# Performance work log

Hardware: AMD Instinct MI355X
Metric: run time of the kernel (lower is better)

## Reference

```python
import jax, jax.numpy as jnp
import numpy as np

B, D, S = 16384, 1024, 2048
LN_EPS = 1e-5


def setup_inputs() -> dict:
    key = jax.random.key(0)
    ks = jax.random.split(key, 16)
    inv_d = 1.0 / np.sqrt(D)
    inv_s = 1.0 / np.sqrt(S)
    inv_ds = 1.0 / np.sqrt(D + S)
    return {
        "x_t": jax.random.normal(ks[0], (B, D), jnp.float32),
        "state": jax.random.normal(ks[1], (B, S), jnp.float32),
        "conditioning": jax.random.normal(ks[2], (B, D), jnp.float32),
        "carry_scale": jax.random.uniform(ks[3], (B, S), jnp.float32),
        # Linear weights stored [in, out] (y = x @ W + b); equivalent math to torch's x @ W.T
        "W_step": jax.random.normal(ks[4], (D, S), jnp.float32) * inv_d,
        "b_step": jnp.zeros((S,), jnp.float32),
        "W_cstep": jax.random.normal(ks[5], (D, S), jnp.float32) * inv_d,
        "W_in": jax.random.normal(ks[6], (D, S), jnp.float32) * inv_d,
        "b_in": jnp.zeros((S,), jnp.float32),
        "W_cin": jax.random.normal(ks[7], (D, S), jnp.float32) * inv_d,
        "W_state": jax.random.normal(ks[8], (S, S), jnp.float32) * inv_s,
        "W_out": jax.random.normal(ks[9], (D + S, D), jnp.float32) * inv_ds,
        "b_out": jnp.zeros((D,), jnp.float32),
        "ln_w": jnp.ones((D,), jnp.float32),
        "ln_b": jnp.zeros((D,), jnp.float32),
        "log_decay": jnp.zeros((S,), jnp.float32),
    }


def reference(x_t, state, conditioning, carry_scale,
              W_step, b_step, W_cstep, W_in, b_in, W_cin,
              W_state, W_out, b_out, ln_w, ln_b, log_decay):
    # input-conditioned step size
    step = jax.nn.softplus(x_t @ W_step + b_step)
    step = step + 0.1 * jax.nn.softplus(conditioning @ W_cstep)
    # candidate state
    proposal = jnp.tanh(x_t @ W_in + b_in + conditioning @ W_cin + state @ W_state)
    # diagonal decay gate
    decay = jnp.exp(-step * jnp.exp(log_decay)) * carry_scale
    new_state = decay * state + (1.0 - decay) * proposal
    # output projection + residual LayerNorm
    out = jnp.concatenate([x_t, new_state], axis=-1) @ W_out + b_out
    h = out + x_t
    mu = jnp.mean(h, axis=-1, keepdims=True)
    var = jnp.mean(jnp.square(h - mu), axis=-1, keepdims=True)
    output = (h - mu) * jax.lax.rsqrt(var + LN_EPS) * ln_w + ln_b
    return output, new_state
```

## Files before the change

kernel.cpp:

```cpp
#include <hip/hip_runtime.h>
#include <hip/hip_bf16.h>
#include <cstdint>
#include <cstddef>

#define BB 16384
#define DD 1024
#define SS 2048

typedef __attribute__((ext_vector_type(8))) short s8vec;
typedef __attribute__((ext_vector_type(4))) short s4vec;
typedef __attribute__((ext_vector_type(4))) float f4vec;

static __device__ __forceinline__ short f2bf(float x) {
  __hip_bfloat16 h = __float2bfloat16(x);
  union { __hip_bfloat16 b; short s; } u; u.b = h; return u.s;
}

static __device__ __forceinline__ float softplus_f(float x) {
  return (x > 20.f) ? x : log1pf(expf(x));
}

static __device__ __forceinline__ void gload16(const void* g, void* l) {
  __builtin_amdgcn_global_load_lds((__attribute__((address_space(1))) void*)g,
                                   (__attribute__((address_space(3))) void*)l,
                                   16, 0, 0);
}

struct EpiParams {
  float* out;
  const float* bias;
  const float* step;
  const float* state;
  const float* carry;
  const float* ldec;
  float* out_state;
  short* xy;
  const float* x;
};

template<int EPI>
__global__ __launch_bounds__(256)
void gemm_bt(const short* __restrict__ A, int lda,
             const short* __restrict__ Bt, int ldb,
             int K, EpiParams ep)
{
  __shared__ short Alds[128 * 32];
  __shared__ short Blds[128 * 32];

  const int tid  = threadIdx.x;
  const int lane = tid & 63;
  const int wv   = tid >> 6;
  const int bm   = blockIdx.y;
  const int bn   = blockIdx.x;

  const int srow = wv * 32 + (lane >> 2);
  const int scol = (lane & 3) * 8;
  const short* Ag = A  + (size_t)(bm * 128 + srow) * lda + scol;
  const short* Bg = Bt + (size_t)(bn * 128 + srow) * ldb + scol;
  short* Al = &Alds[(wv * 32) * 32] + lane * 8;
  short* Bl = &Blds[(wv * 32) * 32] + lane * 8;

  const int wM = (wv >> 1) * 64;
  const int wN = (wv & 1) * 64;
  const int frow = lane & 15;
  const int fk   = (lane >> 4) * 8;

  f4vec acc[4][4];
#pragma unroll
  for (int i = 0; i < 4; i++)
#pragma unroll
    for (int j = 0; j < 4; j++) acc[i][j] = (f4vec){0.f, 0.f, 0.f, 0.f};

  for (int k0 = 0; k0 < K; k0 += 32) {
    __syncthreads();
    gload16(Ag + k0,            Al);
    gload16(Ag + k0 + 16 * lda, Al + 16 * 32);
    gload16(Bg + k0,            Bl);
    gload16(Bg + k0 + 16 * ldb, Bl + 16 * 32);
    __syncthreads();

    s8vec a[4], b[4];
#pragma unroll
    for (int i = 0; i < 4; i++)
      a[i] = *(const s8vec*)&Alds[(wM + i * 16 + frow) * 32 + fk];
#pragma unroll
    for (int j = 0; j < 4; j++)
      b[j] = *(const s8vec*)&Blds[(wN + j * 16 + frow) * 32 + fk];

#pragma unroll
    for (int i = 0; i < 4; i++)
#pragma unroll
      for (int j = 0; j < 4; j++)
        acc[i][j] = __builtin_amdgcn_mfma_f32_16x16x32_bf16(a[i], b[j], acc[i][j], 0, 0, 0);
  }

  const int erow = bm * 128 + wM + (lane >> 4) * 4;
  const int ecol = bn * 128 + wN + (lane & 15);

#pragma unroll
  for (int i = 0; i < 4; i++) {
#pragma unroll
    for (int j = 0; j < 4; j++) {
      const int col = ecol + j * 16;
#pragma unroll
      for (int r = 0; r < 4; r++) {
        const int row = erow + i * 16 + r;
        const float v = acc[i][j][r];
        if constexpr (EPI == 0) {
          ep.out[(size_t)row * SS + col] = softplus_f(v + ep.bias[col]);
        } else if constexpr (EPI == 1) {
          const size_t idx = (size_t)row * SS + col;
          ep.out[idx] = ep.out[idx] + 0.1f * softplus_f(v);
        } else if constexpr (EPI == 2) {
          const size_t idx = (size_t)row * SS + col;
          const float step = ep.step[idx];
          const float dec  = expf(-step * expf(ep.ldec[col])) * ep.carry[idx];
          const float prop = tanhf(v + ep.bias[col]);
          const float ns   = dec * ep.state[idx] + (1.f - dec) * prop;
          ep.out_state[idx] = ns;
          ep.xy[(size_t)row * 3072 + 1024 + col] = f2bf(ns);
        } else {
          const size_t idx = (size_t)row * DD + col;
          ep.out[idx] = v + ep.bias[col] + ep.x[idx];
        }
      }
    }
  }
}

__global__ __launch_bounds__(256)
void tcast(const float* __restrict__ src, int R, int C,
           short* __restrict__ dst, int ldd, int co)
{
  __shared__ float tile[32][33];
  const int c0 = blockIdx.x * 32;
  const int r0 = blockIdx.y * 32;
  const int tx = threadIdx.x;
  const int ty = threadIdx.y;
#pragma unroll
  for (int i = 0; i < 4; i++)
    tile[ty * 4 + i][tx] = src[(size_t)(r0 + ty * 4 + i) * C + c0 + tx];
  __syncthreads();
#pragma unroll
  for (int i = 0; i < 4; i++)
    dst[(size_t)(c0 + ty * 4 + i) * ldd + co + r0 + tx] = f2bf(tile[tx][ty * 4 + i]);
}

__global__ __launch_bounds__(256)
void cast_xc(const float4* __restrict__ x, const float4* __restrict__ c,
             short* __restrict__ Xcat, short* __restrict__ XY)
{
  const size_t i = (size_t)blockIdx.x * 256 + threadIdx.x;
  if (i >= (size_t)BB * (DD / 4)) return;
  const size_t row = i >> 8;
  const int col4 = (int)(i & 255);
  const float4 xv = x[i];
  const float4 cv = c[i];
  const s4vec xs = { f2bf(xv.x), f2bf(xv.y), f2bf(xv.z), f2bf(xv.w) };
  const s4vec cs = { f2bf(cv.x), f2bf(cv.y), f2bf(cv.z), f2bf(cv.w) };
  *(s4vec*)&Xcat[row * 4096 + col4 * 4]        = xs;
  *(s4vec*)&Xcat[row * 4096 + 1024 + col4 * 4] = cs;
  *(s4vec*)&XY[row * 3072 + col4 * 4]          = xs;
}

__global__ __launch_bounds__(256)
void cast_state(const float4* __restrict__ s, short* __restrict__ Xcat)
{
  const size_t i = (size_t)blockIdx.x * 256 + threadIdx.x;
  if (i >= (size_t)BB * (SS / 4)) return;
  const size_t row = i >> 9;
  const int col4 = (int)(i & 511);
  const float4 sv = s[i];
  const s4vec ss = { f2bf(sv.x), f2bf(sv.y), f2bf(sv.z), f2bf(sv.w) };
  *(s4vec*)&Xcat[row * 4096 + 2048 + col4 * 4] = ss;
}

__global__ __launch_bounds__(256)
void ln_kernel(const float* __restrict__ h, const float* __restrict__ w,
               const float* __restrict__ b, float* __restrict__ out)
{
  const int row = blockIdx.x;
  const int t = threadIdx.x;
  const float4 v = ((const float4*)(h + (size_t)row * DD))[t];
  float s  = v.x + v.y + v.z + v.w;
  float sq = v.x * v.x + v.y * v.y + v.z * v.z + v.w * v.w;
#pragma unroll
  for (int off = 32; off; off >>= 1) {
    s  += __shfl_down(s, off);
    sq += __shfl_down(sq, off);
  }
  __shared__ float ss[4], ssq[4];
  const int lane = t & 63, wv = t >> 6;
  if (lane == 0) { ss[wv] = s; ssq[wv] = sq; }
  __syncthreads();
  const float st  = ss[0] + ss[1] + ss[2] + ss[3];
  const float sqt = ssq[0] + ssq[1] + ssq[2] + ssq[3];
  const float mu  = st * (1.f / (float)DD);
  const float var = sqt * (1.f / (float)DD) - mu * mu;
  const float rstd = rsqrtf(var + 1e-5f);
  const float4 wv4 = ((const float4*)w)[t];
  const float4 bv4 = ((const float4*)b)[t];
  float4 o;
  o.x = (v.x - mu) * rstd * wv4.x + bv4.x;
  o.y = (v.y - mu) * rstd * wv4.y + bv4.y;
  o.z = (v.z - mu) * rstd * wv4.z + bv4.z;
  o.w = (v.w - mu) * rstd * wv4.w + bv4.w;
  ((float4*)(out + (size_t)row * DD))[t] = o;
}

extern "C" void kernel_launch(void* const* d_in, const int* in_sizes, int n_in,
                              void* d_out, int out_size, void* d_ws, size_t ws_size,
                              hipStream_t stream)
{
  const float* x_t    = (const float*)d_in[0];
  const float* state  = (const float*)d_in[1];
  const float* cond   = (const float*)d_in[2];
  const float* carry  = (const float*)d_in[3];
  const float* W_step = (const float*)d_in[4];
  const float* b_step = (const float*)d_in[5];
  const float* W_cstep= (const float*)d_in[6];
  const float* W_in   = (const float*)d_in[7];
  const float* b_in   = (const float*)d_in[8];
  const float* W_cin  = (const float*)d_in[9];
  const float* W_state= (const float*)d_in[10];
  const float* W_out  = (const float*)d_in[11];
  const float* b_out  = (const float*)d_in[12];
  const float* ln_w   = (const float*)d_in[13];
  const float* ln_b   = (const float*)d_in[14];
  const float* ldec   = (const float*)d_in[15];

  char* ws = (char*)d_ws;
  size_t off = 0;
  short* Xcat = (short*)(ws + off); off += (size_t)BB * 4096 * 2;
  short* XY   = (short*)(ws + off); off += (size_t)BB * 3072 * 2;
  float* A1   = (float*)(ws + off); off += (size_t)BB * SS * 4;
  short* WstepT  = (short*)(ws + off); off += (size_t)SS * DD * 2;
  short* WcstepT = (short*)(ws + off); off += (size_t)SS * DD * 2;
  short* WcatT   = (short*)(ws + off); off += (size_t)SS * 4096 * 2;
  short* WoutT   = (short*)(ws + off); off += (size_t)DD * 3072 * 2;
  float* hbuf = A1;

  float* out_ln    = (float*)d_out;
  float* out_state = (float*)d_out + (size_t)BB * DD;

  cast_xc<<<dim3(BB * (DD / 4) / 256), 256, 0, stream>>>(
      (const float4*)x_t, (const float4*)cond, Xcat, XY);
  cast_state<<<dim3(BB * (SS / 4) / 256), 256, 0, stream>>>(
      (const float4*)state, Xcat);

  tcast<<<dim3(SS / 32, DD / 32), dim3(32, 8), 0, stream>>>(W_step, DD, SS, WstepT, DD, 0);
  tcast<<<dim3(SS / 32, DD / 32), dim3(32, 8), 0, stream>>>(W_cstep, DD, SS, WcstepT, DD, 0);
  tcast<<<dim3(SS / 32, DD / 32), dim3(32, 8), 0, stream>>>(W_in,   DD, SS, WcatT, 4096, 0);
  tcast<<<dim3(SS / 32, DD / 32), dim3(32, 8), 0, stream>>>(W_cin,  DD, SS, WcatT, 4096, 1024);
  tcast<<<dim3(SS / 32, SS / 32), dim3(32, 8), 0, stream>>>(W_state, SS, SS, WcatT, 4096, 2048);
  tcast<<<dim3(DD / 32, 3072 / 32), dim3(32, 8), 0, stream>>>(W_out, 3072, DD, WoutT, 3072, 0);

  const dim3 gS(SS / 128, BB / 128);
  const dim3 gD(DD / 128, BB / 128);

  EpiParams p1{}; p1.out = A1; p1.bias = b_step;
  gemm_bt<0><<<gS, 256, 0, stream>>>(Xcat, 4096, WstepT, DD, DD, p1);

  EpiParams p2{}; p2.out = A1;
  gemm_bt<1><<<gS, 256, 0, stream>>>(Xcat + 1024, 4096, WcstepT, DD, DD, p2);

  EpiParams p3{};
  p3.bias = b_in; p3.step = A1; p3.state = state; p3.carry = carry;
  p3.ldec = ldec; p3.out_state = out_state; p3.xy = XY;
  gemm_bt<2><<<gS, 256, 0, stream>>>(Xcat, 4096, WcatT, 4096, 4096, p3);

  EpiParams p4{}; p4.out = hbuf; p4.bias = b_out; p4.x = x_t;
  gemm_bt<3><<<gD, 256, 0, stream>>>(XY, 3072, WoutT, 3072, 3072, p4);

  ln_kernel<<<dim3(BB), 256, 0, stream>>>(hbuf, ln_w, ln_b, out_ln);
}
```

Baseline: 1.906 ms.

## Replace 128x128 GEMM with 256x256 double-buffered swizzled-LDS pipelined kernel

Replaces the simple 128x128 bf16 MFMA GEMM, which synchronised twice per K=32 step, with a 256x256 tile kernel using 512 threads and K=64 stages. The new kernel double-buffers LDS with XOR-swizzled layout and interleaves global-to-LDS loads with MFMA quarters under explicit waitcnt, barriers and setprio. The goal is more data reuse per tile, fewer bank conflicts and overlap of memory with compute. In exchange it uses much more LDS and more registers per thread, which lowers occupancy, and it relies on a hand-written schedule that is fragile to get right.

```diff
diff --git a/kernel.cpp b/kernel.cpp
--- a/kernel.cpp
+++ b/kernel.cpp
@@ -38,74 +38,153 @@
   const float* x;
 };
 
+#define BAR() do { asm volatile("" ::: "memory"); __builtin_amdgcn_s_barrier(); asm volatile("" ::: "memory"); } while (0)
+#define WAIT_LGKM0() do { asm volatile("s_waitcnt lgkmcnt(0)" ::: "memory"); __builtin_amdgcn_sched_barrier(0); } while (0)
+#define WAIT_VM(n)   do { asm volatile("s_waitcnt vmcnt(" #n ")" ::: "memory"); __builtin_amdgcn_sched_barrier(0); } while (0)
+
 template<int EPI>
-__global__ __launch_bounds__(256)
-void gemm_bt(const short* __restrict__ A, int lda,
+__global__ __launch_bounds__(512, 2)
+void gemm256(const short* __restrict__ A, int lda,
              const short* __restrict__ Bt, int ldb,
-             int K, EpiParams ep)
-{
-  __shared__ short Alds[128 * 32];
-  __shared__ short Blds[128 * 32];
+             int K, int nbxl, EpiParams ep)
+{
+  __shared__ short lds0[65536];
 
   const int tid  = threadIdx.x;
   const int lane = tid & 63;
-  const int wv   = tid >> 6;
-  const int bm   = blockIdx.y;
-  const int bn   = blockIdx.x;
-
-  const int srow = wv * 32 + (lane >> 2);
-  const int scol = (lane & 3) * 8;
-  const short* Ag = A  + (size_t)(bm * 128 + srow) * lda + scol;
-  const short* Bg = Bt + (size_t)(bn * 128 + srow) * ldb + scol;
-  short* Al = &Alds[(wv * 32) * 32] + lane * 8;
-  short* Bl = &Blds[(wv * 32) * 32] + lane * 8;
-
-  const int wM = (wv >> 1) * 64;
-  const int wN = (wv & 1) * 64;
+  const int w    = tid >> 6;
+  const int wm   = w >> 2;
+  const int wn   = w & 3;
   const int frow = lane & 15;
-  const int fk   = (lane >> 4) * 8;
-
-  f4vec acc[4][4];
-#pragma unroll
-  for (int i = 0; i < 4; i++)
+  const int klane = lane >> 4;
+  const int swb  = lane & 7;
+
+  const int lin = blockIdx.x;
+  const int bm  = lin >> nbxl;
+  const int bn  = lin & ((1 << nbxl) - 1);
+
+  const int rl0    = w * 16 + (lane >> 3);
+  const int colsw8 = ((lane & 7) ^ ((lane >> 3) & 7)) * 8;
+  const int dOff   = w * 1024 + lane * 8;
+
+  const short* gA0 = A  + (size_t)(bm * 256 +       rl0) * lda + colsw8;
+  const short* gA1 = A  + (size_t)(bm * 256 + 128 + rl0) * lda + colsw8;
+  const short* gB0 = Bt + (size_t)(bn * 256 +       rl0) * ldb + colsw8;
+  const short* gB1 = Bt + (size_t)(bn * 256 + 128 + rl0) * ldb + colsw8;
+  const int kmax = K - 64;
+
+  auto STAGE = [&](int buf, int h, int kt) {
+    const short* g = (h == 0) ? gA0 : (h == 1) ? gA1 : (h == 2) ? gB0 : gB1;
+    const int ld = (h < 2) ? lda : ldb;
+    int kk = kt * 64; if (kk > kmax) kk = kmax;
+    short* d = &lds0[buf * 32768 + h * 8192 + dOff];
+    gload16(g + kk,                 d);
+    gload16(g + kk + (size_t)8 * ld, d + 512);
+  };
+
+  auto LDA2 = [&](int buf, int frp, s8vec (&a)[2][2]) {
+    const short* base = &lds0[buf * 32768 + wm * 8192];
+#pragma unroll
+    for (int i = 0; i < 2; i++) {
+      const int row = (frp * 2 + i) * 16 + frow;
+#pragma unroll
+      for (int ks = 0; ks < 2; ks++) {
+        const int slot = (ks * 4 + klane) ^ swb;
+        a[i][ks] = *(const s8vec*)&base[row * 64 + slot * 8];
+      }
+    }
+  };
+
+  auto LDB8 = [&](int buf, s8vec (&b)[4][2]) {
+    const short* base = &lds0[buf * 32768 + 16384 + (wn >> 1) * 8192];
+#pragma unroll
+    for (int fc = 0; fc < 4; fc++) {
+      const int row = (wn & 1) * 64 + fc * 16 + frow;
+#pragma unroll
+      for (int ks = 0; ks < 2; ks++) {
+        const int slot = (ks * 4 + klane) ^ swb;
+        b[fc][ks] = *(const s8vec*)&base[row * 64 + slot * 8];
+      }
+    }
+  };
+
+  f4vec acc[8][4];
+#pragma unroll
+  for (int i = 0; i < 8; i++)
 #pragma unroll
     for (int j = 0; j < 4; j++) acc[i][j] = (f4vec){0.f, 0.f, 0.f, 0.f};
 
-  for (int k0 = 0; k0 < K; k0 += 32) {
-    __syncthreads();
-    gload16(Ag + k0,            Al);
-    gload16(Ag + k0 + 16 * lda, Al + 16 * 32);
-    gload16(Bg + k0,            Bl);
-    gload16(Bg + k0 + 16 * ldb, Bl + 16 * 32);
-    __syncthreads();
-
-    s8vec a[4], b[4];
-#pragma unroll
-    for (int i = 0; i < 4; i++)
-      a[i] = *(const s8vec*)&Alds[(wM + i * 16 + frow) * 32 + fk];
-#pragma unroll
-    for (int j = 0; j < 4; j++)
-      b[j] = *(const s8vec*)&Blds[(wN + j * 16 + frow) * 32 + fk];
-
-#pragma unroll
-    for (int i = 0; i < 4; i++)
-#pragma unroll
-      for (int j = 0; j < 4; j++)
-        acc[i][j] = __builtin_amdgcn_mfma_f32_16x16x32_bf16(a[i], b[j], acc[i][j], 0, 0, 0);
+  s8vec aX[2][2], aY[2][2], bf0[4][2], bf1[4][2];
+
+#define QMFMA(aS, bS, q) do {                                                  \
+  _Pragma("unroll") for (int i = 0; i < 2; i++)                                \
+  _Pragma("unroll") for (int fc = 0; fc < 4; fc++)                             \
+  _Pragma("unroll") for (int ks = 0; ks < 2; ks++)                             \
+    acc[(q) * 2 + i][fc] = __builtin_amdgcn_mfma_f32_16x16x32_bf16(            \
+        aS[i][ks], bS[fc][ks], acc[(q) * 2 + i][fc], 0, 0, 0);                 \
+} while (0)
+
+  STAGE(0, 0, 0); STAGE(0, 1, 0); STAGE(0, 2, 0); STAGE(0, 3, 0);
+  STAGE(1, 0, 1);
+  WAIT_VM(2);
+  BAR();
+  LDB8(0, bf0);
+  LDA2(0, 0, aX);
+
+  const int J = K >> 7;
+  for (int j = 0; j < J; ++j) {
+    const int t1 = 2 * j + 1, t2 = 2 * j + 2, t3 = 2 * j + 3;
+    LDA2(0, 1, aY); STAGE(1, 1, t1);
+    BAR(); WAIT_LGKM0();
+    __builtin_amdgcn_s_setprio(1); QMFMA(aX, bf0, 0); __builtin_amdgcn_s_setprio(0);
+    BAR();
+    LDA2(0, 2, aX); STAGE(1, 2, t1);
+    BAR(); WAIT_LGKM0();
+    __builtin_amdgcn_s_setprio(1); QMFMA(aY, bf0, 1); __builtin_amdgcn_s_setprio(0);
+    BAR();
+    LDA2(0, 3, aY); STAGE(1, 3, t1);
+    BAR(); WAIT_LGKM0();
+    __builtin_amdgcn_s_setprio(1); QMFMA(aX, bf0, 2); __builtin_amdgcn_s_setprio(0);
+    BAR();
+    STAGE(0, 0, t2);
+    WAIT_VM(2);
+    BAR();
+    LDB8(1, bf1); LDA2(1, 0, aX);
+    __builtin_amdgcn_s_setprio(1); QMFMA(aY, bf0, 3); __builtin_amdgcn_s_setprio(0);
+    BAR();
+    LDA2(1, 1, aY); STAGE(0, 1, t2);
+    BAR(); WAIT_LGKM0();
+    __builtin_amdgcn_s_setprio(1); QMFMA(aX, bf1, 0); __builtin_amdgcn_s_setprio(0);
+    BAR();
+    LDA2(1, 2, aX); STAGE(0, 2, t2);
+    BAR(); WAIT_LGKM0();
+    __builtin_amdgcn_s_setprio(1); QMFMA(aY, bf1, 1); __builtin_amdgcn_s_setprio(0);
+    BAR();
+    LDA2(1, 3, aY); STAGE(0, 3, t2);
+    BAR(); WAIT_LGKM0();
+    __builtin_amdgcn_s_setprio(1); QMFMA(aX, bf1, 2); __builtin_amdgcn_s_setprio(0);
+    BAR();
+    STAGE(1, 0, t3);
+    WAIT_VM(2);
+    BAR();
+    LDB8(0, bf0); LDA2(0, 0, aX);
+    __builtin_amdgcn_s_setprio(1); QMFMA(aY, bf1, 3); __builtin_amdgcn_s_setprio(0);
+    BAR();
   }
-
-  const int erow = bm * 128 + wM + (lane >> 4) * 4;
-  const int ecol = bn * 128 + wN + (lane & 15);
-
-#pragma unroll
-  for (int i = 0; i < 4; i++) {
-#pragma unroll
-    for (int j = 0; j < 4; j++) {
-      const int col = ecol + j * 16;
+  asm volatile("s_waitcnt vmcnt(0) lgkmcnt(0)" ::: "memory");
+
+  const int r0 = bm * 256 + wm * 128 + (lane >> 4) * 4;
+  const int c0 = bn * 256 + wn * 64 + (lane & 15);
+
+#pragma unroll
+  for (int fr = 0; fr < 8; fr++) {
+#pragma unroll
+    for (int fc = 0; fc < 4; fc++) {
+      const int col = c0 + fc * 16;
 #pragma unroll
       for (int r = 0; r < 4; r++) {
-        const int row = erow + i * 16 + r;
-        const float v = acc[i][j][r];
+        const int row = r0 + fr * 16 + r;
+        const float v = acc[fr][fc][r];
         if constexpr (EPI == 0) {
           ep.out[(size_t)row * SS + col] = softplus_f(v + ep.bias[col]);
         } else if constexpr (EPI == 1) {
@@ -126,6 +205,7 @@
       }
     }
   }
+#undef QMFMA
 }
 
 __global__ __launch_bounds__(256)
@@ -255,22 +335,22 @@
   tcast<<<dim3(SS / 32, SS / 32), dim3(32, 8), 0, stream>>>(W_state, SS, SS, WcatT, 4096, 2048);
   tcast<<<dim3(DD / 32, 3072 / 32), dim3(32, 8), 0, stream>>>(W_out, 3072, DD, WoutT, 3072, 0);
 
-  const dim3 gS(SS / 128, BB / 128);
-  const dim3 gD(DD / 128, BB / 128);
+  const int nwgS = (BB / 256) * (SS / 256);
+  const int nwgD = (BB / 256) * (DD / 256);
 
   EpiParams p1{}; p1.out = A1; p1.bias = b_step;
-  gemm_bt<0><<<gS, 256, 0, stream>>>(Xcat, 4096, WstepT, DD, DD, p1);
+  gemm256<0><<<dim3(nwgS), 512, 0, stream>>>(Xcat, 4096, WstepT, DD, 1024, 3, p1);
 
   EpiParams p2{}; p2.out = A1;
-  gemm_bt<1><<<gS, 256, 0, stream>>>(Xcat + 1024, 4096, WcstepT, DD, DD, p2);
+  gemm256<1><<<dim3(nwgS), 512, 0, stream>>>(Xcat + 1024, 4096, WcstepT, DD, 1024, 3, p2);
 
   EpiParams p3{};
   p3.bias = b_in; p3.step = A1; p3.state = state; p3.carry = carry;
   p3.ldec = ldec; p3.out_state = out_state; p3.xy = XY;
-  gemm_bt<2><<<gS, 256, 0, stream>>>(Xcat, 4096, WcatT, 4096, 4096, p3);
+  gemm256<2><<<dim3(nwgS), 512, 0, stream>>>(Xcat, 4096, WcatT, 4096, 4096, 3, p3);
 
   EpiParams p4{}; p4.out = hbuf; p4.bias = b_out; p4.x = x_t;
-  gemm_bt<3><<<gD, 256, 0, stream>>>(XY, 3072, WoutT, 3072, 3072, p4);
+  gemm256<3><<<dim3(nwgD), 512, 0, stream>>>(XY, 3072, WoutT, 3072, 3072, 2, p4);
 
   ln_kernel<<<dim3(BB), 256, 0, stream>>>(hbuf, ln_w, ln_b, out_ln);
 }
```

Result: faster. 1.576 ms (-17.3%).
